# Kernel optimization log

Measured on AMD Instinct MI355X. Metric: run time of the kernel, lower is better.

## Reference

```python
import jax, jax.numpy as jnp
import numpy as np

N = 4_194_304          # number of rays
DAMPING = 0.5          # LM(0.5)
MAX_DELTA = 1000.0     # clamp on LM step
N_ITER = 30            # no_grad warmup iterations
XMIN, XMAX, TAU = -1.0, 1.0, 1.0


def _surface_F(pts, c):
    # implicit parabolic rod: F(p) = x - c*(y^2 + z^2); pts: [N,3]
    return pts[..., 0] - c * (pts[..., 1] ** 2 + pts[..., 2] ** 2)


def _lm_delta(P, V, t, c):
    # Levenberg-Marquardt step for f(t) = F(P + t*V):
    # delta = f * f' / (f'^2 + damping), clamped to [-max_delta, max_delta]
    pts = P + t[:, None] * V                     # [N,3]
    f = _surface_F(pts, c)                       # [N]
    # f'(t) = gradF(pts) . V, gradF = (1, -2c*y, -2c*z)
    fp = V[:, 0] - 2.0 * c * (pts[:, 1] * V[:, 1] + pts[:, 2] * V[:, 2])
    delta = f * fp / (fp * fp + DAMPING)
    return jnp.clip(delta, -MAX_DELTA, MAX_DELTA)


def setup_inputs() -> dict:
    key = jax.random.key(0)
    k1, k2 = jax.random.split(key, 2)
    P = jax.random.normal(k1, (N, 3), jnp.float32) * 2.0
    V = jax.random.normal(k2, (N, 3), jnp.float32)
    V = V / jnp.linalg.norm(V, axis=-1, keepdims=True)
    a, b = 0.3, -0.2
    Rz = jnp.array([[np.cos(a), -np.sin(a), 0.0],
                    [np.sin(a),  np.cos(a), 0.0],
                    [0.0,        0.0,       1.0]], jnp.float32)
    Ry = jnp.array([[np.cos(b), 0.0, np.sin(b)],
                    [0.0,       1.0, 0.0],
                    [-np.sin(b), 0.0, np.cos(b)]], jnp.float32)
    R = Rz @ Ry                                  # rigid rotation [3,3]
    T = jnp.array([0.1, -0.2, 0.05], jnp.float32)
    c = jnp.float32(0.05)
    loss_in = jnp.float32(0.0)
    return {"P": P, "V": V, "R": R, "T": T, "c": c, "loss_in": loss_in}


def reference(P, V, R, T, c, loss_in):
    n = P.shape[0]
    # transform.inverse_points / inverse_vectors: R^T (p - T), R^T v
    P_local = (P - T) @ R                        # [N,3]
    V_local = V @ R                              # [N,3]

    # 30 no-grad LM iterations (torch.no_grad -> stop_gradient on inputs)
    Pl = jax.lax.stop_gradient(P_local)
    Vl = jax.lax.stop_gradient(V_local)
    cs = jax.lax.stop_gradient(c)

    def body(i, t):
        return t - _lm_delta(Pl, Vl, t, cs)

    t0 = jax.lax.fori_loop(0, N_ITER, body, jnp.zeros((n,), jnp.float32))

    # final differentiable LM step
    t = t0 - _lm_delta(P_local, V_local, t0, c)

    points_local = P_local + t[:, None] * V_local
    scale = jnp.mean(jnp.abs(jnp.array([XMIN, XMAX, TAU], jnp.float32)))
    F = _surface_F(points_local, c) / scale
    loss = loss_in + jnp.sum(F ** 2) / n
    return loss
```

## Files before the change

### kernel.cpp

```cpp
#include <hip/hip_runtime.h>


#define LM_ITERS 31
constexpr float DAMPING   = 0.5f;
constexpr float MAX_DELTA = 1000.0f;

__global__ __launch_bounds__(256) void rod_kernel(
    const float* __restrict__ P, const float* __restrict__ V,
    const float* __restrict__ Rm, const float* __restrict__ Tv,
    const float* __restrict__ c_ptr, double* __restrict__ ws, int n)
{
    const float c  = c_ptr[0];
    const float r00 = Rm[0], r01 = Rm[1], r02 = Rm[2];
    const float r10 = Rm[3], r11 = Rm[4], r12 = Rm[5];
    const float r20 = Rm[6], r21 = Rm[7], r22 = Rm[8];
    const float t0 = Tv[0], t1 = Tv[1], t2 = Tv[2];

    const int tid  = blockIdx.x * blockDim.x + threadIdx.x;
    const int base = tid * 4;

    double acc = 0.0;
    if (base < n) {
        const float4* P4 = (const float4*)P;
        const float4* V4 = (const float4*)V;
        float4 pa = P4[tid * 3 + 0], pb = P4[tid * 3 + 1], pcv = P4[tid * 3 + 2];
        float4 va = V4[tid * 3 + 0], vb = V4[tid * 3 + 1], vcv = V4[tid * 3 + 2];

        const float px[4] = {pa.x, pa.w, pb.z, pcv.y};
        const float py[4] = {pa.y, pb.x, pb.w, pcv.z};
        const float pz[4] = {pa.z, pb.y, pcv.x, pcv.w};
        const float vx[4] = {va.x, va.w, vb.z, vcv.y};
        const float vy[4] = {va.y, vb.x, vb.w, vcv.z};
        const float vz[4] = {va.z, vb.y, vcv.x, vcv.w};

        float A[4], A2[4], B[4], C[4], tt[4];
        #pragma unroll
        for (int r = 0; r < 4; ++r) {
            const float qx = px[r] - t0, qy = py[r] - t1, qz = pz[r] - t2;
            const float plx = qx * r00 + qy * r10 + qz * r20;
            const float ply = qx * r01 + qy * r11 + qz * r21;
            const float plz = qx * r02 + qy * r12 + qz * r22;
            const float vlx = vx[r] * r00 + vy[r] * r10 + vz[r] * r20;
            const float vly = vx[r] * r01 + vy[r] * r11 + vz[r] * r21;
            const float vlz = vx[r] * r02 + vy[r] * r12 + vz[r] * r22;
            A[r]  = -c * (vly * vly + vlz * vlz);
            B[r]  = vlx - 2.0f * c * (ply * vly + plz * vlz);
            C[r]  = plx - c * (ply * ply + plz * plz);
            A2[r] = A[r] + A[r];
            tt[r] = 0.0f;
        }

        #pragma unroll 1
        for (int it = 0; it < LM_ITERS; ++it) {
            #pragma unroll
            for (int r = 0; r < 4; ++r) {
                const float fp  = fmaf(A2[r], tt[r], B[r]);
                const float f   = fmaf(fmaf(A[r], tt[r], B[r]), tt[r], C[r]);
                const float den = fmaf(fp, fp, DAMPING);
                const float num = f * fp;
                float delta = num * __builtin_amdgcn_rcpf(den);
                delta = fminf(fmaxf(delta, -MAX_DELTA), MAX_DELTA);
                tt[r] -= delta;
            }
        }

        #pragma unroll
        for (int r = 0; r < 4; ++r) {
            if (base + r < n) {
                const float f = fmaf(fmaf(A[r], tt[r], B[r]), tt[r], C[r]);
                acc += (double)(f * f);
            }
        }
    }

    for (int off = 32; off > 0; off >>= 1)
        acc += __shfl_down(acc, off, 64);
    __shared__ double sacc[4];
    const int lane = threadIdx.x & 63, wave = threadIdx.x >> 6;
    if (lane == 0) sacc[wave] = acc;
    __syncthreads();
    if (threadIdx.x == 0) {
        atomicAdd(ws, sacc[0] + sacc[1] + sacc[2] + sacc[3]);
    }
}

__global__ void rod_finalize(const double* __restrict__ ws,
                             const float* __restrict__ loss_in,
                             float* __restrict__ out, double inv_n)
{
    out[0] = (float)(ws[0] * inv_n + (double)loss_in[0]);
}

extern "C" void kernel_launch(void* const* d_in, const int* in_sizes, int n_in,
                              void* d_out, int out_size, void* d_ws, size_t ws_size,
                              hipStream_t stream) {
    const float* P       = (const float*)d_in[0];
    const float* V       = (const float*)d_in[1];
    const float* R       = (const float*)d_in[2];
    const float* T       = (const float*)d_in[3];
    const float* c       = (const float*)d_in[4];
    const float* loss_in = (const float*)d_in[5];

    const int n = in_sizes[0] / 3;

    hipMemsetAsync(d_ws, 0, sizeof(double), stream);

    const int threads = (n + 3) / 4;
    const int block   = 256;
    const int grid    = (threads + block - 1) / block;
    rod_kernel<<<grid, block, 0, stream>>>(P, V, R, T, c, (double*)d_ws, n);
    rod_finalize<<<1, 1, 0, stream>>>((const double*)d_ws, loss_in,
                                      (float*)d_out, 1.0 / (double)n);
}
```

Baseline: 163.5 us.

## Track f and f' incrementally with packed float2 math, 8 rays per thread, fused finalize

The LM iteration now updates f and f' incrementally from the step d, instead of re-evaluating the quadratic in t. The math is done on packed 2-wide float vectors so the compiler can emit packed FMA/mul instructions. Each thread handles 8 rays with 6 float4 loads, and the tail is handled in a scalar path. The separate finalize kernel is replaced by a last-block-done counter that writes the output inside the main kernel. Incremental updates can accumulate rounding differently from direct evaluation, and halving the thread count reduces the parallelism available for latency hiding.

```diff
diff --git a/kernel.cpp b/kernel.cpp
--- a/kernel.cpp
+++ b/kernel.cpp
@@ -5,10 +5,18 @@
 constexpr float DAMPING   = 0.5f;
 constexpr float MAX_DELTA = 1000.0f;
 
+typedef float v2f __attribute__((ext_vector_type(2)));
+
+static __device__ __forceinline__ v2f vfma(v2f a, v2f b, v2f c) {
+    return __builtin_elementwise_fma(a, b, c);
+}
+
 __global__ __launch_bounds__(256) void rod_kernel(
     const float* __restrict__ P, const float* __restrict__ V,
     const float* __restrict__ Rm, const float* __restrict__ Tv,
-    const float* __restrict__ c_ptr, double* __restrict__ ws, int n)
+    const float* __restrict__ c_ptr, const float* __restrict__ loss_in,
+    double* __restrict__ ws, float* __restrict__ out,
+    int n, double inv_n)
 {
     const float c  = c_ptr[0];
     const float r00 = Rm[0], r01 = Rm[1], r02 = Rm[2];
@@ -17,59 +25,87 @@
     const float t0 = Tv[0], t1 = Tv[1], t2 = Tv[2];
 
     const int tid  = blockIdx.x * blockDim.x + threadIdx.x;
-    const int base = tid * 4;
+    const int base = tid * 8;
 
     double acc = 0.0;
-    if (base < n) {
+    if (base + 8 <= n) {
+        union { float4 q[6]; float s[24]; } up, uv;
         const float4* P4 = (const float4*)P;
         const float4* V4 = (const float4*)V;
-        float4 pa = P4[tid * 3 + 0], pb = P4[tid * 3 + 1], pcv = P4[tid * 3 + 2];
-        float4 va = V4[tid * 3 + 0], vb = V4[tid * 3 + 1], vcv = V4[tid * 3 + 2];
+        #pragma unroll
+        for (int i = 0; i < 6; ++i) { up.q[i] = P4[tid * 6 + i]; uv.q[i] = V4[tid * 6 + i]; }
 
-        const float px[4] = {pa.x, pa.w, pb.z, pcv.y};
-        const float py[4] = {pa.y, pb.x, pb.w, pcv.z};
-        const float pz[4] = {pa.z, pb.y, pcv.x, pcv.w};
-        const float vx[4] = {va.x, va.w, vb.z, vcv.y};
-        const float vy[4] = {va.y, vb.x, vb.w, vcv.z};
-        const float vz[4] = {va.z, vb.y, vcv.x, vcv.w};
-
-        float A[4], A2[4], B[4], C[4], tt[4];
+        v2f nA[4], nA2[4], f[4], fp[4];
         #pragma unroll
-        for (int r = 0; r < 4; ++r) {
-            const float qx = px[r] - t0, qy = py[r] - t1, qz = pz[r] - t2;
+        for (int r = 0; r < 8; ++r) {
+            const float qx = up.s[3 * r + 0] - t0;
+            const float qy = up.s[3 * r + 1] - t1;
+            const float qz = up.s[3 * r + 2] - t2;
+            const float vx = uv.s[3 * r + 0], vy = uv.s[3 * r + 1], vz = uv.s[3 * r + 2];
             const float plx = qx * r00 + qy * r10 + qz * r20;
             const float ply = qx * r01 + qy * r11 + qz * r21;
             const float plz = qx * r02 + qy * r12 + qz * r22;
-            const float vlx = vx[r] * r00 + vy[r] * r10 + vz[r] * r20;
-            const float vly = vx[r] * r01 + vy[r] * r11 + vz[r] * r21;
-            const float vlz = vx[r] * r02 + vy[r] * r12 + vz[r] * r22;
-            A[r]  = -c * (vly * vly + vlz * vlz);
-            B[r]  = vlx - 2.0f * c * (ply * vly + plz * vlz);
-            C[r]  = plx - c * (ply * ply + plz * plz);
-            A2[r] = A[r] + A[r];
-            tt[r] = 0.0f;
+            const float vlx = vx * r00 + vy * r10 + vz * r20;
+            const float vly = vx * r01 + vy * r11 + vz * r21;
+            const float vlz = vx * r02 + vy * r12 + vz * r22;
+            const float A  = -c * (vly * vly + vlz * vlz);
+            const float B  = vlx - 2.0f * c * (ply * vly + plz * vlz);
+            const float C  = plx - c * (ply * ply + plz * plz);
+            const int j = r >> 1, k = r & 1;
+            nA[j][k]  = -A;
+            nA2[j][k] = -2.0f * A;
+            f[j][k]   = C;
+            fp[j][k]  = B;
         }
+
+        const v2f vdamp = {DAMPING, DAMPING};
+        const v2f vlo   = {-MAX_DELTA, -MAX_DELTA};
+        const v2f vhi   = { MAX_DELTA,  MAX_DELTA};
 
         #pragma unroll 1
         for (int it = 0; it < LM_ITERS; ++it) {
             #pragma unroll
-            for (int r = 0; r < 4; ++r) {
-                const float fp  = fmaf(A2[r], tt[r], B[r]);
-                const float f   = fmaf(fmaf(A[r], tt[r], B[r]), tt[r], C[r]);
-                const float den = fmaf(fp, fp, DAMPING);
-                const float num = f * fp;
-                float delta = num * __builtin_amdgcn_rcpf(den);
-                delta = fminf(fmaxf(delta, -MAX_DELTA), MAX_DELTA);
-                tt[r] -= delta;
+            for (int j = 0; j < 4; ++j) {
+                const v2f den = vfma(fp[j], fp[j], vdamp);
+                v2f rcp;
+                rcp.x = __builtin_amdgcn_rcpf(den.x);
+                rcp.y = __builtin_amdgcn_rcpf(den.y);
+                const v2f num = f[j] * fp[j];
+                v2f d = num * rcp;
+                d = __builtin_elementwise_min(__builtin_elementwise_max(d, vlo), vhi);
+                const v2f tmp = vfma(nA[j], d, fp[j]);
+                f[j]  = vfma(-d, tmp, f[j]);
+                fp[j] = vfma(nA2[j], d, fp[j]);
             }
         }
 
         #pragma unroll
-        for (int r = 0; r < 4; ++r) {
-            if (base + r < n) {
-                const float f = fmaf(fmaf(A[r], tt[r], B[r]), tt[r], C[r]);
-                acc += (double)(f * f);
+        for (int j = 0; j < 4; ++j) {
+            acc += (double)f[j].x * (double)f[j].x;
+            acc += (double)f[j].y * (double)f[j].y;
+        }
+    } else if (base < n) {
+        for (int r = base; r < n; ++r) {
+            const float qx = P[3 * r + 0] - t0, qy = P[3 * r + 1] - t1, qz = P[3 * r + 2] - t2;
+            const float vx = V[3 * r + 0], vy = V[3 * r + 1], vz = V[3 * r + 2];
+            const float ply = qx * r01 + qy * r11 + qz * r21;
+            const float plz = qx * r02 + qy * r12 + qz * r22;
+            const float plx = qx * r00 + qy * r10 + qz * r20;
+            const float vlx = vx * r00 + vy * r10 + vz * r20;
+            const float vly = vx * r01 + vy * r11 + vz * r21;
+            const float vlz = vx * r02 + vy * r12 + vz * r22;
+            const float A = -c * (vly * vly + vlz * vlz);
+            float fpv = vlx - 2.0f * c * (ply * vly + plz * vlz);
+            float fv  = plx - c * (ply * ply + plz * plz);
+            for (int it = 0; it < LM_ITERS; ++it) {
+                const float den = fmaf(fpv, fpv, DAMPING);
+                float d = fv * fpv * __builtin_amdgcn_rcpf(den);
+                d = fminf(fmaxf(d, -MAX_DELTA), MAX_DELTA);
+                const float tmp = fmaf(-A, d, fpv);
+                fv  = fmaf(-d, tmp, fv);
+                fpv = fmaf(-2.0f * A, d, fpv);
             }
+            acc += (double)fv * (double)fv;
         }
     }
 
@@ -80,15 +116,16 @@
     if (lane == 0) sacc[wave] = acc;
     __syncthreads();
     if (threadIdx.x == 0) {
-        atomicAdd(ws, sacc[0] + sacc[1] + sacc[2] + sacc[3]);
+        double* ws_acc = ws;
+        unsigned int* ws_cnt = (unsigned int*)(ws + 1);
+        atomicAdd(ws_acc, sacc[0] + sacc[1] + sacc[2] + sacc[3]);
+        __threadfence();
+        const unsigned int old = atomicAdd(ws_cnt, 1u);
+        if (old == gridDim.x - 1) {
+            const double total = atomicAdd(ws_acc, 0.0);
+            out[0] = (float)(total * inv_n + (double)loss_in[0]);
+        }
     }
-}
-
-__global__ void rod_finalize(const double* __restrict__ ws,
-                             const float* __restrict__ loss_in,
-                             float* __restrict__ out, double inv_n)
-{
-    out[0] = (float)(ws[0] * inv_n + (double)loss_in[0]);
 }
 
 extern "C" void kernel_launch(void* const* d_in, const int* in_sizes, int n_in,
@@ -103,12 +140,12 @@
 
     const int n = in_sizes[0] / 3;
 
-    hipMemsetAsync(d_ws, 0, sizeof(double), stream);
+    hipMemsetAsync(d_ws, 0, 16, stream);
 
-    const int threads = (n + 3) / 4;
+    const int threads = (n + 7) / 8;
     const int block   = 256;
     const int grid    = (threads + block - 1) / block;
-    rod_kernel<<<grid, block, 0, stream>>>(P, V, R, T, c, (double*)d_ws, n);
-    rod_finalize<<<1, 1, 0, stream>>>((const double*)d_ws, loss_in,
-                                      (float*)d_out, 1.0 / (double)n);
+    rod_kernel<<<grid, block, 0, stream>>>(P, V, R, T, c, loss_in,
+                                           (double*)d_ws, (float*)d_out,
+                                           n, 1.0 / (double)n);
 }
```

Result: slower. 219.2 us (+34.0%).
